# Optimization experiments

Hardware: AMD Instinct MI355X
Metric: run time of the kernel (lower is better)

## Reference

```python
import jax, jax.numpy as jnp
import numpy as np

N, E, D, L = 50000, 625000, 128, 7
EPS = 1e-7   # GENConv message epsilon
T = 1.0      # softmax aggregation temperature (learn_t=False)
NUM_ATOM_FEATS, ATOM_VOCAB = 9, 64
NUM_BOND_FEATS, BOND_VOCAB = 3, 8


def setup_inputs() -> dict:
    key = jax.random.key(0)
    ks = jax.random.split(key, 9)
    x = jax.random.randint(ks[0], (N, NUM_ATOM_FEATS), 0, ATOM_VOCAB, dtype=jnp.int32)
    edge_index = jax.random.randint(ks[1], (2, E), 0, N, dtype=jnp.int32)
    edge_attr = jax.random.randint(ks[2], (E, NUM_BOND_FEATS), 0, BOND_VOCAB, dtype=jnp.int32)
    atom_emb = jax.random.normal(ks[3], (NUM_ATOM_FEATS, ATOM_VOCAB, D), dtype=jnp.float32) * 0.1
    bond_emb = jax.random.normal(ks[4], (NUM_BOND_FEATS, BOND_VOCAB, D), dtype=jnp.float32) * 0.1
    W = jax.random.normal(ks[5], (L, D, D), dtype=jnp.float32) / np.sqrt(D).astype(np.float32)
    b = jnp.zeros((L, D), dtype=jnp.float32)
    ln_gamma = jnp.ones((L, D), dtype=jnp.float32)
    ln_beta = jnp.zeros((L, D), dtype=jnp.float32)
    return dict(x=x, edge_index=edge_index, edge_attr=edge_attr,
                atom_emb=atom_emb, bond_emb=bond_emb, W=W, b=b,
                ln_gamma=ln_gamma, ln_beta=ln_beta)


def _layer_norm(h, g, bta):
    mu = jnp.mean(h, axis=-1, keepdims=True)
    var = jnp.var(h, axis=-1, keepdims=True)
    return (h - mu) * jax.lax.rsqrt(var + 1e-5) * g + bta


def _gen_conv(h, src, dst, edge_emb, Wl, bl):
    # GENConv: msg = relu(x_j + e) + eps; softmax aggregation over dst; Linear(x + m)
    msg = jax.nn.relu(h[src] + edge_emb) + EPS                 # [E, D]
    logits = msg * T
    seg_max = jax.ops.segment_max(logits, dst, num_segments=N)  # [N, D]
    seg_max = jnp.where(jnp.isfinite(seg_max), seg_max, 0.0)    # empty segments
    e = jnp.exp(logits - seg_max[dst])                          # [E, D]
    denom = jax.ops.segment_sum(e, dst, num_segments=N)         # [N, D]
    alpha = e / (denom[dst] + 1e-16)
    m = jax.ops.segment_sum(alpha * msg, dst, num_segments=N)   # [N, D]
    return (h + m) @ Wl + bl


def reference(x, edge_index, edge_attr, atom_emb, bond_emb, W, b, ln_gamma, ln_beta):
    src, dst = edge_index[0], edge_index[1]
    # AtomEncoder: sum of per-feature embedding lookups -> [N, D]
    h = jnp.sum(atom_emb[jnp.arange(NUM_ATOM_FEATS)[None, :], x], axis=1)
    # BondEncoder (conv_encode_edge=False: encoded once) -> [E, D]
    edge_emb = jnp.sum(bond_emb[jnp.arange(NUM_BOND_FEATS)[None, :], edge_attr], axis=1)
    # res+ block, dropout=0 (no-op)
    h = _gen_conv(h, src, dst, edge_emb, W[0], b[0])
    for layer in range(1, L):
        h2 = jax.nn.relu(_layer_norm(h, ln_gamma[layer - 1], ln_beta[layer - 1]))
        h = _gen_conv(h2, src, dst, edge_emb, W[layer], b[layer]) + h
    h = _layer_norm(h, ln_gamma[L - 1], ln_beta[L - 1])
    return h
```

## Files before the change

### kernel.cpp

```cpp
#include <hip/hip_runtime.h>
#include <hip/hip_fp16.h>
#include <math.h>


constexpr int D = 128;
constexpr int NA = 9;
constexpr int NB = 3;
constexpr float L2E = 1.4426950408889634f;
constexpr float INV_L2E = 0.6931471805599453f;

using half8  = __attribute__((ext_vector_type(8))) _Float16;
using h2v    = __attribute__((ext_vector_type(2))) _Float16;
using floatx4 = __attribute__((ext_vector_type(4))) float;


__global__ void k_setup0(const float* __restrict__ bemb, __half* __restrict__ comb16,
                         const float* __restrict__ W, __half* __restrict__ Wt16,
                         int* __restrict__ deg, int* __restrict__ dbin,
                         int* __restrict__ dcur, int4* __restrict__ meta,
                         unsigned* __restrict__ recs1,
                         int N, int N4, int wtot, int E) {
    int gid = blockIdx.x * 256 + threadIdx.x;
    if (gid < N) deg[gid] = 0;
    if (gid < 64) { dbin[gid] = 0; dcur[gid] = 0; recs1[E + gid] = 0; }
    if (gid >= N && gid < N4) meta[gid] = make_int4(0, 0, -1, 0);
    if (gid < 512 * 32) {
        int c = gid >> 5, q = gid & 31;
        int a0 = c >> 6, a1 = (c >> 3) & 7, a2 = c & 7;
        float4 v0 = *(const float4*)(bemb + (a0)*D + q * 4);
        float4 v1 = *(const float4*)(bemb + (8 + a1) * D + q * 4);
        float4 v2 = *(const float4*)(bemb + (16 + a2) * D + q * 4);
        __half2* c2 = (__half2*)comb16;
        c2[c * 64 + q * 2]     = __floats2half2_rn(L2E * (v0.x + v1.x + v2.x),
                                                   L2E * (v0.y + v1.y + v2.y));
        c2[c * 64 + q * 2 + 1] = __floats2half2_rn(L2E * (v0.z + v1.z + v2.z),
                                                   L2E * (v0.w + v1.w + v2.w));
    }
    if (gid < wtot) {
        int l = gid >> 14;
        int rem = gid & 16383;
        int f = rem >> 7, k = rem & 127;
        Wt16[gid] = __float2half_rn(W[(l << 14) + k * 128 + f]);
    }
}


__global__ void k_hist(const int* __restrict__ dst, int* __restrict__ deg, int E) {
    int e = blockIdx.x * 256 + threadIdx.x;
    if (e < E) atomicAdd(&deg[dst[e]], 1);
}

__global__ void k_scan_a(const int* __restrict__ deg, int* __restrict__ offs,
                         int* __restrict__ bsum, int N) {
    __shared__ int s[256];
    int i = blockIdx.x * 256 + threadIdx.x;
    int v = (i < N) ? deg[i] : 0;
    s[threadIdx.x] = v;
    __syncthreads();
    for (int d = 1; d < 256; d <<= 1) {
        int add = (threadIdx.x >= d) ? s[threadIdx.x - d] : 0;
        __syncthreads();
        s[threadIdx.x] += add;
        __syncthreads();
    }
    if (i < N) offs[i + 1] = s[threadIdx.x];
    if (threadIdx.x == 255) bsum[blockIdx.x] = s[255];
    if (i == 0) offs[0] = 0;
}

__global__ void k_scan_b(const int* __restrict__ bsum, int* __restrict__ bexc, int nb) {
    __shared__ int s[256];
    int t = threadIdx.x;
    int v = (t < nb) ? bsum[t] : 0;
    s[t] = v;
    __syncthreads();
    for (int d = 1; d < 256; d <<= 1) {
        int add = (t >= d) ? s[t - d] : 0;
        __syncthreads();
        s[t] += add;
        __syncthreads();
    }
    if (t < nb) bexc[t] = s[t] - v;
}

__global__ void k_scan_c_dhist(int* __restrict__ offs, const int* __restrict__ bexc,
                               const int* __restrict__ deg, int* __restrict__ dbin,
                               int N) {
    __shared__ int lb[64];
    int t = threadIdx.x;
    if (t < 64) lb[t] = 0;
    __syncthreads();
    int i = blockIdx.x * 256 + t;
    if (i < N) {
        offs[i + 1] += bexc[blockIdx.x];
        int d = deg[i]; d = d < 63 ? d : 63;
        atomicAdd(&lb[63 - d], 1);
    }
    __syncthreads();
    if (t < 64 && lb[t] > 0) atomicAdd(&dbin[t], lb[t]);
}

__global__ void k_fill(const int* __restrict__ src, const int* __restrict__ dst,
                       const int* __restrict__ attr, int* __restrict__ offs,
                       unsigned* __restrict__ recs1,
                       const int* __restrict__ dbin, int* __restrict__ doff, int E) {
    int e = blockIdx.x * 256 + threadIdx.x;
    if (e < E) {
        int d = dst[e];
        int pos = atomicAdd(&offs[d], 1);
        unsigned cidx = (unsigned)(attr[e * 3] * 64 + attr[e * 3 + 1] * 8 + attr[e * 3 + 2]);
        recs1[pos] = (unsigned)src[e] | (cidx << 17);
    }
    if (blockIdx.x == 0 && threadIdx.x == 0) {
        int acc = 0;
        for (int b = 0; b < 64; ++b) { doff[b] = acc; acc += dbin[b]; }
    }
}


__global__ void k_dfill_atom(const int* __restrict__ deg, const int* __restrict__ doff,
                             int* __restrict__ dcur, const int* __restrict__ offs,
                             int4* __restrict__ meta,
                             const int* __restrict__ x, const float* __restrict__ aemb,
                             __half* __restrict__ h16, int N, int nbl) {
    if ((int)blockIdx.x < nbl) {
        __shared__ int lc[64], lbase[64];
        int t = threadIdx.x;
        if (t < 64) lc[t] = 0;
        __syncthreads();
        int i = blockIdx.x * 256 + t;
        int b = 0, rank = 0;
        if (i < N) {
            int d = deg[i]; d = d < 63 ? d : 63;
            b = 63 - d;
            rank = atomicAdd(&lc[b], 1);
        }
        __syncthreads();
        if (t < 64 && lc[t] > 0) lbase[t] = atomicAdd(&dcur[t], lc[t]);
        __syncthreads();
        if (i < N) {
            int su = (i > 0) ? offs[i - 1] : 0;
            int eu = offs[i];
            meta[doff[b] + lbase[b] + rank] = make_int4(su, eu, i, 0);
        }
    }
    int wid = (blockIdx.x * blockDim.x + threadIdx.x) >> 6;
    int lane = threadIdx.x & 63;
    if (wid >= N) return;
    const int* xr = x + wid * NA;
    float ax = 0.f, ay = 0.f;
#pragma unroll
    for (int f = 0; f < NA; ++f) {
        int v = xr[f];
        const float2 e = *(const float2*)(aemb + (f * 64 + v) * D + 2 * lane);
        ax += e.x; ay += e.y;
    }
    ((__half2*)h16)[wid * 64 + lane] = __floats2half2_rn(ax * L2E, ay * L2E);
}


__global__ __launch_bounds__(256) void k_agg(const __half* __restrict__ h16,
                      const unsigned* __restrict__ recs1,
                      const int4* __restrict__ meta,
                      const __half* __restrict__ comb16,
                      __half* __restrict__ t16, int N) {
    int w = (blockIdx.x * blockDim.x + threadIdx.x) >> 6;
    int lane = threadIdx.x & 63;
    int base = w * 4;
    if (base >= N) return;

    const h2v* hrow = (const h2v*)h16 + lane;
    const h2v* crow = (const h2v*)comb16 + lane;
    const h2v zero2 = (h2v)(_Float16)0;

    int4 m0 = meta[base], m1 = meta[base + 1], m2 = meta[base + 2], m3 = meta[base + 3];
    int su0 = __builtin_amdgcn_readfirstlane(m0.x), eu0 = __builtin_amdgcn_readfirstlane(m0.y), nid0 = __builtin_amdgcn_readfirstlane(m0.z);
    int su1 = __builtin_amdgcn_readfirstlane(m1.x), eu1 = __builtin_amdgcn_readfirstlane(m1.y), nid1 = __builtin_amdgcn_readfirstlane(m1.z);
    int su2 = __builtin_amdgcn_readfirstlane(m2.x), eu2 = __builtin_amdgcn_readfirstlane(m2.y), nid2 = __builtin_amdgcn_readfirstlane(m2.z);
    int su3 = __builtin_amdgcn_readfirstlane(m3.x), eu3 = __builtin_amdgcn_readfirstlane(m3.y), nid3 = __builtin_amdgcn_readfirstlane(m3.z);

    unsigned rv0 = 0, rv1 = 0, rv2 = 0, rv3 = 0;
    if (su0 < eu0) rv0 = recs1[su0 + lane];
    if (su1 < eu1) rv1 = recs1[su1 + lane];
    if (su2 < eu2) rv2 = recs1[su2 + lane];
    if (su3 < eu3) rv3 = recs1[su3 + lane];

    auto process = [&](int su, int eu, int nid, unsigned recv) {
        if (nid < 0) return;
        h2v hm2 = hrow[nid * 64];
        if (su >= eu) {
            ((__half2*)t16)[nid * 64 + lane] = __floats2half2_rn(
                (float)hm2[0] * INV_L2E, (float)hm2[1] * INV_L2E);
            return;
        }
        float Sx = 0.f, Sy = 0.f, Wx = 0.f, Wy = 0.f;
        h2v hq[16], cq[16];
        int e0 = su;
        for (;;) {
            int lastc = (eu < e0 + 48) ? eu : e0 + 48;

            auto load4 = [&](int b2, int slot) {
#pragma unroll
                for (int i = 0; i < 4; ++i) {
                    unsigned r = __builtin_amdgcn_readlane(recv, b2 + i - e0);
                    int sj = (int)(r & 0x1FFFFu);
                    int cj = (int)(r >> 17);
                    hq[slot * 4 + i] = hrow[sj * 64];
                    cq[slot * 4 + i] = crow[cj * 64];
                }
            };
            auto comp4u = [&](int slot) {
#pragma unroll
                for (int i = 0; i < 4; ++i) {
                    h2v m = hq[slot * 4 + i] + cq[slot * 4 + i];
                    m = __builtin_elementwise_max(m, zero2);
                    float u0 = (float)m[0], u1 = (float)m[1];
                    float px = __builtin_amdgcn_exp2f(u0);
                    float py = __builtin_amdgcn_exp2f(u1);
                    Sx += px; Sy += py;
                    Wx = fmaf(px, u0, Wx);
                    Wy = fmaf(py, u1, Wy);
                }
            };
            auto comp4m = [&](int gb, int slot) {
#pragma unroll
                for (int i = 0; i < 4; ++i) {
                    h2v m = hq[slot * 4 + i] + cq[slot * 4 + i];
                    m = __builtin_elementwise_max(m, zero2);
                    float u0 = (float)m[0], u1 = (float)m[1];
                    bool valid = (gb + i) < lastc;
                    float px = valid ? __builtin_amdgcn_exp2f(u0) : 0.f;
                    float py = valid ? __builtin_amdgcn_exp2f(u1) : 0.f;
                    Sx += px; Sy += py;
                    Wx = fmaf(px, u0, Wx);
                    Wy = fmaf(py, u1, Wy);
                }
            };

            load4(e0, 0);
            if (e0 + 4  < lastc) load4(e0 + 4, 1);
            if (e0 + 8  < lastc) load4(e0 + 8, 2);
            if (e0 + 12 < lastc) load4(e0 + 12, 3);

            int e = e0;
            for (; e + 16 < lastc; e += 16) {
                comp4u(0); load4(e + 16, 0);
                comp4u(1); load4(e + 20, 1);
                comp4u(2); load4(e + 24, 2);
                comp4u(3); load4(e + 28, 3);
            }
            comp4m(e, 0);
            if (e + 4  < lastc) comp4m(e + 4, 1);
            if (e + 8  < lastc) comp4m(e + 8, 2);
            if (e + 12 < lastc) comp4m(e + 12, 3);

            e0 = lastc;
            if (e0 >= eu) break;
            recv = recs1[e0 + lane];
        }

        float tx = ((float)hm2[0] + Wx / (Sx + 1e-16f)) * INV_L2E;
        float ty = ((float)hm2[1] + Wy / (Sy + 1e-16f)) * INV_L2E;
        ((__half2*)t16)[nid * 64 + lane] = __floats2half2_rn(tx, ty);
    };

    process(su0, eu0, nid0, rv0);
    process(su1, eu1, nid1, rv1);
    process(su2, eu2, nid2, rv2);
    process(su3, eu3, nid3, rv3);
}


template <int MODE>
__global__ __launch_bounds__(256) void k_gemm(const __half* __restrict__ A16,
                                              const __half* __restrict__ Wt16,
                                              const float* __restrict__ bl,
                                              const __half* __restrict__ res16,
                                              __half* __restrict__ hres16,
                                              const float* __restrict__ g,
                                              const float* __restrict__ bta,
                                              __half* __restrict__ h16,
                                              float* __restrict__ out,
                                              int N, int useRes) {
    __shared__ float2 sm[2][2][16];
    int lane = threadIdx.x & 63;
    int wave = threadIdx.x >> 6;
    int grp = wave >> 1, half = wave & 1;
    int quad = lane >> 4, col = lane & 15;
    int node = blockIdx.x * 32 + grp * 16 + col;
    bool nok = node < N;
    int nc = nok ? node : N - 1;

    const __half* arow = A16 + (size_t)nc * 128;
    half8 bfrag[4];
#pragma unroll
    for (int ks = 0; ks < 4; ++ks)
        bfrag[ks] = *(const half8*)(arow + ks * 32 + quad * 8);

    uint2 rr[4];
    if (useRes) {
#pragma unroll
        for (int ft2 = 0; ft2 < 4; ++ft2) {
            int f0 = (half * 4 + ft2) * 16 + quad * 4;
            rr[ft2] = *(const uint2*)(res16 + (size_t)nc * 128 + f0);
        }
    }

    floatx4 acc[4];
#pragma unroll
    for (int ft2 = 0; ft2 < 4; ++ft2) acc[ft2] = (floatx4){0.f, 0.f, 0.f, 0.f};

#pragma unroll
    for (int ft2 = 0; ft2 < 4; ++ft2) {
        const __half* wrow = Wt16 + (size_t)((half * 4 + ft2) * 16 + col) * 128;
#pragma unroll
        for (int ks = 0; ks < 4; ++ks) {
            half8 afrag = *(const half8*)(wrow + ks * 32 + quad * 8);
            acc[ft2] = __builtin_amdgcn_mfma_f32_16x16x32_f16(afrag, bfrag[ks],
                                                              acc[ft2], 0, 0, 0);
        }
    }

    float s = 0.f, ss = 0.f;
#pragma unroll
    for (int ft2 = 0; ft2 < 4; ++ft2) {
        int f0 = (half * 4 + ft2) * 16 + quad * 4;
        float4 bb = *(const float4*)(bl + f0);
        float o0 = acc[ft2][0] + bb.x, o1 = acc[ft2][1] + bb.y;
        float o2 = acc[ft2][2] + bb.z, o3 = acc[ft2][3] + bb.w;
        if (useRes) {
            __half2 r01 = *(__half2*)&rr[ft2].x, r23 = *(__half2*)&rr[ft2].y;
            o0 += __low2float(r01); o1 += __high2float(r01);
            o2 += __low2float(r23); o3 += __high2float(r23);
        }
        acc[ft2][0] = o0; acc[ft2][1] = o1; acc[ft2][2] = o2; acc[ft2][3] = o3;
        s += (o0 + o1) + (o2 + o3);
        ss += fmaf(o0, o0, o1 * o1) + fmaf(o2, o2, o3 * o3);
        if (MODE == 0 && nok) {
            __half2 h01 = __floats2half2_rn(o0, o1);
            __half2 h23 = __floats2half2_rn(o2, o3);
            uint2 pk = make_uint2(*(unsigned*)&h01, *(unsigned*)&h23);
            *(uint2*)(hres16 + (size_t)node * 128 + f0) = pk;
        }
    }
    s += __shfl_xor(s, 16, 64);  ss += __shfl_xor(ss, 16, 64);
    s += __shfl_xor(s, 32, 64);  ss += __shfl_xor(ss, 32, 64);
    if (quad == 0) sm[grp][half][col] = make_float2(s, ss);
    __syncthreads();
    float2 oth = sm[grp][half ^ 1][col];
    float st = s + oth.x, sst = ss + oth.y;
    float mu = st * (1.f / 128.f);
    float var = sst * (1.f / 128.f) - mu * mu;
    float rs = rsqrtf(var + 1e-5f);

#pragma unroll
    for (int ft2 = 0; ft2 < 4; ++ft2) {
        int f0 = (half * 4 + ft2) * 16 + quad * 4;
        float4 gg = *(const float4*)(g + f0);
        float4 bt = *(const float4*)(bta + f0);
        float l0 = (acc[ft2][0] - mu) * rs * gg.x + bt.x;
        float l1 = (acc[ft2][1] - mu) * rs * gg.y + bt.y;
        float l2 = (acc[ft2][2] - mu) * rs * gg.z + bt.z;
        float l3 = (acc[ft2][3] - mu) * rs * gg.w + bt.w;
        if (MODE == 0) {
            l0 = fmaxf(l0, 0.f); l1 = fmaxf(l1, 0.f);
            l2 = fmaxf(l2, 0.f); l3 = fmaxf(l3, 0.f);
            if (nok) {
                __half2 h01 = __floats2half2_rn(l0 * L2E, l1 * L2E);
                __half2 h23 = __floats2half2_rn(l2 * L2E, l3 * L2E);
                uint2 pk = make_uint2(*(unsigned*)&h01, *(unsigned*)&h23);
                *(uint2*)(h16 + (size_t)node * 128 + f0) = pk;
            }
        } else {
            if (nok)
                *(float4*)(out + (size_t)node * 128 + f0) =
                    make_float4(l0, l1, l2, l3);
        }
    }
}


extern "C" void kernel_launch(void* const* d_in, const int* in_sizes, int n_in,
                              void* d_out, int out_size, void* d_ws, size_t ws_size,
                              hipStream_t stream) {
    const int*   x    = (const int*)d_in[0];
    const int*   ei   = (const int*)d_in[1];
    const int*   attr = (const int*)d_in[2];
    const float* aemb = (const float*)d_in[3];
    const float* bemb = (const float*)d_in[4];
    const float* Wf   = (const float*)d_in[5];
    const float* bf   = (const float*)d_in[6];
    const float* gam  = (const float*)d_in[7];
    const float* bet  = (const float*)d_in[8];
    float* out = (float*)d_out;

    const int N = in_sizes[0] / NA;
    const int E = in_sizes[1] / 2;
    const int L = in_sizes[5] / (D * D);
    const int N4 = (N + 3) & ~3;

    char* ws = (char*)d_ws;
    size_t o = 0;
    auto carve = [&](size_t bytes) -> void* {
        void* p = (void*)(ws + o);
        o += (bytes + 255) & ~(size_t)255;
        return p;
    };
    __half* hres16 = (__half*)carve((size_t)N * D * 2);
    __half* h16    = (__half*)carve((size_t)N * D * 2);
    __half* t16    = (__half*)carve((size_t)N * D * 2);
    unsigned* recs1 = (unsigned*)carve((size_t)(E + 64) * 4);
    __half* comb16 = (__half*)carve(512 * D * 2);
    __half* Wt16   = (__half*)carve((size_t)L * D * D * 2);
    int*    deg    = (int*)carve((size_t)N * 4);
    int*    offs   = (int*)carve((size_t)(N + 1) * 4);
    int4*   meta   = (int4*)carve((size_t)N4 * 16);
    int*    dbin   = (int*)carve(256);
    int*    doff   = (int*)carve(256);
    int*    dcur   = (int*)carve(256);
    int*    bsum   = (int*)carve(4096);
    int*    bexc   = (int*)carve(4096);

    const int* src = ei;
    const int* dst = ei + E;

    int ebl = (E + 255) / 256;
    int nbl = (N + 255) / 256;
    int wtot = L * D * D;
    int s0max = wtot > N4 ? wtot : N4;
    int sbl = (s0max + 255) / 256;

    k_setup0<<<sbl, 256, 0, stream>>>(bemb, comb16, Wf, Wt16, deg, dbin, dcur,
                                      meta, recs1, N, N4, wtot, E);
    k_hist<<<ebl, 256, 0, stream>>>(dst, deg, E);
    k_scan_a<<<nbl, 256, 0, stream>>>(deg, offs, bsum, N);
    k_scan_b<<<1, 256, 0, stream>>>(bsum, bexc, nbl);
    k_scan_c_dhist<<<nbl, 256, 0, stream>>>(offs, bexc, deg, dbin, N);
    k_fill<<<ebl, 256, 0, stream>>>(src, dst, attr, offs, recs1, dbin, doff, E);

    int wbl = (N * 64 + 255) / 256;
    k_dfill_atom<<<wbl, 256, 0, stream>>>(deg, doff, dcur, offs, meta,
                                          x, aemb, h16, N, nbl);

    int nwv = N4 / 4;
    int abl = (nwv * 64 + 255) / 256;
    int gbl = (N + 31) / 32;
    for (int l = 0; l < L; ++l) {
        k_agg<<<abl, 256, 0, stream>>>(h16, recs1, meta, comb16, t16, N);
        if (l == L - 1) {
            k_gemm<1><<<gbl, 256, 0, stream>>>(t16, Wt16 + l * D * D, bf + l * D,
                                               hres16, hres16,
                                               gam + l * D, bet + l * D, h16, out,
                                               N, 1);
        } else {
            k_gemm<0><<<gbl, 256, 0, stream>>>(t16, Wt16 + l * D * D, bf + l * D,
                                               hres16, hres16,
                                               gam + l * D, bet + l * D, h16, out,
                                               N, l > 0 ? 1 : 0);
        }
    }
}
```

Measured before the change: 589.4 us.

## Make aggregation persistent and stage bond-embedding table in LDS

The aggregation kernel becomes a persistent grid of 256 blocks with 1024 threads each. Every wave grid-strides over degree-sorted node slots instead of handling a fixed group of four. Each block first copies the combined bond-embedding table (512 rows of 128 halves) into shared memory, so the per-edge embedding gather reads LDS instead of global memory or cache. In exchange it gives up the four-node per-wave interleaving, pays a 128 KB table copy per block per launch, and caps occupancy at one large block per CU. The loop now bounds slots by N rather than the padded count and drops the nid<0 guard, which relies on the meta layout having no padding entries below N.

```diff
diff --git a/kernel.cpp b/kernel.cpp
--- a/kernel.cpp
+++ b/kernel.cpp
@@ -159,62 +159,65 @@
 }
 
 
-__global__ __launch_bounds__(256) void k_agg(const __half* __restrict__ h16,
+__global__ __launch_bounds__(1024, 1) void k_agg(const __half* __restrict__ h16,
                       const unsigned* __restrict__ recs1,
                       const int4* __restrict__ meta,
                       const __half* __restrict__ comb16,
-                      __half* __restrict__ t16, int N) {
-    int w = (blockIdx.x * blockDim.x + threadIdx.x) >> 6;
+                      __half* __restrict__ t16, int N, int nwaves) {
+    extern __shared__ __half combl[];
+    {
+        const uint4* cg = (const uint4*)comb16;
+        uint4* cl = (uint4*)combl;
+#pragma unroll
+        for (int i = 0; i < 8; ++i)
+            cl[threadIdx.x + i * 1024] = cg[threadIdx.x + i * 1024];
+    }
+    __syncthreads();
+
     int lane = threadIdx.x & 63;
-    int base = w * 4;
-    if (base >= N) return;
+    int gw = blockIdx.x * (1024 / 64) + (threadIdx.x >> 6);
 
     const h2v* hrow = (const h2v*)h16 + lane;
-    const h2v* crow = (const h2v*)comb16 + lane;
+    const h2v* crow = (const h2v*)combl + lane;
     const h2v zero2 = (h2v)(_Float16)0;
 
-    int4 m0 = meta[base], m1 = meta[base + 1], m2 = meta[base + 2], m3 = meta[base + 3];
-    int su0 = __builtin_amdgcn_readfirstlane(m0.x), eu0 = __builtin_amdgcn_readfirstlane(m0.y), nid0 = __builtin_amdgcn_readfirstlane(m0.z);
-    int su1 = __builtin_amdgcn_readfirstlane(m1.x), eu1 = __builtin_amdgcn_readfirstlane(m1.y), nid1 = __builtin_amdgcn_readfirstlane(m1.z);
-    int su2 = __builtin_amdgcn_readfirstlane(m2.x), eu2 = __builtin_amdgcn_readfirstlane(m2.y), nid2 = __builtin_amdgcn_readfirstlane(m2.z);
-    int su3 = __builtin_amdgcn_readfirstlane(m3.x), eu3 = __builtin_amdgcn_readfirstlane(m3.y), nid3 = __builtin_amdgcn_readfirstlane(m3.z);
-
-    unsigned rv0 = 0, rv1 = 0, rv2 = 0, rv3 = 0;
-    if (su0 < eu0) rv0 = recs1[su0 + lane];
-    if (su1 < eu1) rv1 = recs1[su1 + lane];
-    if (su2 < eu2) rv2 = recs1[su2 + lane];
-    if (su3 < eu3) rv3 = recs1[su3 + lane];
-
-    auto process = [&](int su, int eu, int nid, unsigned recv) {
-        if (nid < 0) return;
+    h2v hq[16], cq[16];
+
+    for (int slot = gw; slot < N; slot += nwaves) {
+        int4 m = meta[slot];
+        int su = __builtin_amdgcn_readfirstlane(m.x);
+        int eu = __builtin_amdgcn_readfirstlane(m.y);
+        int nid = __builtin_amdgcn_readfirstlane(m.z);
+
         h2v hm2 = hrow[nid * 64];
         if (su >= eu) {
             ((__half2*)t16)[nid * 64 + lane] = __floats2half2_rn(
                 (float)hm2[0] * INV_L2E, (float)hm2[1] * INV_L2E);
-            return;
-        }
+            continue;
+        }
+        unsigned recv = recs1[su + lane];
+
         float Sx = 0.f, Sy = 0.f, Wx = 0.f, Wy = 0.f;
-        h2v hq[16], cq[16];
         int e0 = su;
         for (;;) {
             int lastc = (eu < e0 + 48) ? eu : e0 + 48;
 
-            auto load4 = [&](int b2, int slot) {
+            auto load4 = [&](int b2, int slot2) {
 #pragma unroll
                 for (int i = 0; i < 4; ++i) {
                     unsigned r = __builtin_amdgcn_readlane(recv, b2 + i - e0);
                     int sj = (int)(r & 0x1FFFFu);
                     int cj = (int)(r >> 17);
-                    hq[slot * 4 + i] = hrow[sj * 64];
-                    cq[slot * 4 + i] = crow[cj * 64];
+                    hq[slot2 * 4 + i] = hrow[sj * 64];
+                    cq[slot2 * 4 + i] = crow[cj * 64];
                 }
             };
-            auto comp4u = [&](int slot) {
+            auto comp4u = [&](int slot2) {
 #pragma unroll
                 for (int i = 0; i < 4; ++i) {
-                    h2v m = hq[slot * 4 + i] + cq[slot * 4 + i];
-                    m = __builtin_elementwise_max(m, zero2);
-                    float u0 = (float)m[0], u1 = (float)m[1];
+                    h2v mm = hq[slot2 * 4 + i] + cq[slot2 * 4 + i];
+                    mm = __builtin_elementwise_max(mm, zero2);
+                    float u0 = (float)mm[0], u1 = (float)mm[1];
                     float px = __builtin_amdgcn_exp2f(u0);
                     float py = __builtin_amdgcn_exp2f(u1);
                     Sx += px; Sy += py;
@@ -222,12 +225,12 @@
                     Wy = fmaf(py, u1, Wy);
                 }
             };
-            auto comp4m = [&](int gb, int slot) {
+            auto comp4m = [&](int gb, int slot2) {
 #pragma unroll
                 for (int i = 0; i < 4; ++i) {
-                    h2v m = hq[slot * 4 + i] + cq[slot * 4 + i];
-                    m = __builtin_elementwise_max(m, zero2);
-                    float u0 = (float)m[0], u1 = (float)m[1];
+                    h2v mm = hq[slot2 * 4 + i] + cq[slot2 * 4 + i];
+                    mm = __builtin_elementwise_max(mm, zero2);
+                    float u0 = (float)mm[0], u1 = (float)mm[1];
                     bool valid = (gb + i) < lastc;
                     float px = valid ? __builtin_amdgcn_exp2f(u0) : 0.f;
                     float py = valid ? __builtin_amdgcn_exp2f(u1) : 0.f;
@@ -262,12 +265,7 @@
         float tx = ((float)hm2[0] + Wx / (Sx + 1e-16f)) * INV_L2E;
         float ty = ((float)hm2[1] + Wy / (Sy + 1e-16f)) * INV_L2E;
         ((__half2*)t16)[nid * 64 + lane] = __floats2half2_rn(tx, ty);
-    };
-
-    process(su0, eu0, nid0, rv0);
-    process(su1, eu1, nid1, rv1);
-    process(su2, eu2, nid2, rv2);
-    process(su3, eu3, nid3, rv3);
+    }
 }
 
 
@@ -442,11 +440,12 @@
     k_dfill_atom<<<wbl, 256, 0, stream>>>(deg, doff, dcur, offs, meta,
                                           x, aemb, h16, N, nbl);
 
-    int nwv = N4 / 4;
-    int abl = (nwv * 64 + 255) / 256;
+    const int ablocks = 256;
+    const int nwaves = ablocks * (1024 / 64);
     int gbl = (N + 31) / 32;
     for (int l = 0; l < L; ++l) {
-        k_agg<<<abl, 256, 0, stream>>>(h16, recs1, meta, comb16, t16, N);
+        k_agg<<<ablocks, 1024, 512 * D * 2, stream>>>(h16, recs1, meta, comb16,
+                                                      t16, N, nwaves);
         if (l == L - 1) {
             k_gemm<1><<<gbl, 256, 0, stream>>>(t16, Wt16 + l * D * D, bf + l * D,
                                                hres16, hres16,
```

Result: slower. 663.0 us (+12.5%).
